# Performance work log

Measured on AMD Instinct MI355X. Metric: run time of the kernel, lower is better.

The kernel has to match this reference:

```python
import jax, jax.numpy as jnp
import numpy as np

HS = 512

def setup_inputs() -> dict:
    key = jax.random.key(0)
    k1, k2, k3, k4 = jax.random.split(key, 4)
    B, T, D = 128, 1024, 256
    x = jax.random.normal(k1, (B, T, D), dtype=jnp.float32)
    # init like torch.Tensor (uninitialized) -> use small random values for a usable baseline
    W = jax.random.normal(k2, (D, 4 * HS), dtype=jnp.float32) * (1.0 / np.sqrt(D))
    U = jax.random.normal(k3, (HS, 4 * HS), dtype=jnp.float32) * (1.0 / np.sqrt(HS))
    bias = jax.random.normal(k4, (4 * HS,), dtype=jnp.float32) * 0.01
    return {"x": x, "W": W, "U": U, "bias": bias}

def reference(x, W, U, bias):
    B = x.shape[0]
    h0 = jnp.zeros((B, HS), dtype=x.dtype)
    c0 = jnp.zeros((B, HS), dtype=x.dtype)
    # precompute input projection for all timesteps (same math, hoisted out of recurrence)
    xW = jnp.einsum('btd,dg->btg', x, W) + bias  # [B, T, 4*HS]

    def step(carry, xw_t):
        h_t, c_t = carry
        gates = xw_t + h_t @ U  # [B, 4*HS]
        i_t = jax.nn.sigmoid(gates[:, :HS])
        f_t = jax.nn.sigmoid(gates[:, HS:2 * HS])
        g_t = jnp.tanh(gates[:, 2 * HS:3 * HS])
        o_t = jax.nn.sigmoid(gates[:, 3 * HS:])
        c_t = f_t * c_t + i_t * g_t
        h_t = o_t * jnp.tanh(c_t)
        return (h_t, c_t), h_t

    (h_T, c_T), hs = jax.lax.scan(step, (h0, c0), jnp.swapaxes(xW, 0, 1))
    hidden_sequence = jnp.swapaxes(hs, 0, 1)  # [B, T, HS]
    return hidden_sequence, (h_T, c_T)
```

## Files before the change

### kernel.cpp

```cpp
#include <hip/hip_runtime.h>

typedef __attribute__((ext_vector_type(8))) short short8;
typedef __attribute__((ext_vector_type(4))) float floatx4;

#define B_   128
#define T_   1024
#define D_   256
#define HS_  512
#define NKT  24

#define OFF_X   0ull
#define SZ_X    ((size_t)B_*T_*D_*2)
#define OFF_W   (OFF_X + SZ_X)
#define SZ_W    ((size_t)16*4*48*64*8*2)
#define OFF_H   (OFF_W + SZ_W)
#define SZ_H    ((size_t)2*B_*HS_*2)
#define OFF_C   (OFF_H + SZ_H)

__device__ inline unsigned short f2bf(float f){
  union { float f; unsigned u; } v; v.f = f;
  unsigned r = v.u + 0x7FFFu + ((v.u >> 16) & 1u);
  return (unsigned short)(r >> 16);
}

__global__ void k_zero(unsigned* __restrict__ hbuf32, unsigned* __restrict__ cnt32){
  int i = blockIdx.x*256 + threadIdx.x;
  if (i < (int)(SZ_H/4)) hbuf32[i] = 0u;
  if (i < 512)           cnt32[i]  = 0u;
}

__global__ void k_convx(const float* __restrict__ x, unsigned short* __restrict__ xb){
  size_t i = ((size_t)blockIdx.x*256 + threadIdx.x)*8;
  const float* s = x + i;
  short8 r;
#pragma unroll
  for (int j=0;j<8;j++) r[j] = (short)f2bf(s[j]);
  *(short8*)(void*)(xb + i) = r;
}

__global__ void k_wfrag(const float* __restrict__ W, const float* __restrict__ U,
                        unsigned short* __restrict__ wf){
  int flat = blockIdx.x*256 + threadIdx.x;
  int lane = flat & 63;
  int rest = flat >> 6;
  int nt   = rest & 1;
  int kt   = (rest >> 1) % 24;
  int sw   = (rest >> 1) / 24;
  int w    = sw & 3;
  int sub  = sw >> 2;
  int colg  = w*HS_ + sub*32 + nt*16 + (lane & 15);
  int kbase = kt*32 + (lane >> 4)*8;
  short8 r;
#pragma unroll
  for (int j=0;j<8;j++){
    int k = kbase + j;
    float v = (k < D_) ? W[(size_t)k*2048 + colg] : U[(size_t)(k-D_)*2048 + colg];
    r[j] = (short)f2bf(v);
  }
  *(short8*)(void*)(wf + (size_t)flat*8) = r;
}

__global__ __launch_bounds__(256, 1) void k_lstm(
  const unsigned short* __restrict__ xb,
  const unsigned short* __restrict__ wf,
  const float* __restrict__ bias,
  unsigned short* __restrict__ hbuf,
  unsigned int* __restrict__ cnt,
  float* __restrict__ out)
{
  __shared__ unsigned short A_lds[NKT*64*8];
  __shared__ float g_lds[4][16][34];

  const int wg   = blockIdx.x;
  const int group = wg >> 4, sub = wg & 15;
  const int tid  = threadIdx.x;
  const int wave = tid >> 6, lane = tid & 63;

  short8 bw[48];
  {
    const unsigned short* wp = wf + (size_t)(sub*4 + wave)*48*512 + (size_t)lane*8;
#pragma unroll
    for (int i=0;i<48;i++) bw[i] = *(const short8*)(const void*)(wp + i*512);
  }

  const int row_e = tid >> 4;
  const int cp    = (tid & 15)*2;
  float bres[8];
#pragma unroll
  for (int q=0;q<4;q++)
#pragma unroll
    for (int e=0;e<2;e++)
      bres[q*2+e] = bias[q*HS_ + sub*32 + cp + e];

  float c0 = 0.f, c1 = 0.f;
  unsigned int* mycnt = cnt + group*64;
  const size_t HSQ = (size_t)B_*T_*HS_;
  const int grow = group*16 + row_e;
  const int gcol = sub*32 + cp;

  const int xrow0 = (tid >> 5);
  const int xkc   = (tid & 31);
  short8 xr0, xr1;
  {
    const unsigned short* s0 = xb + ((size_t)(group*16 + xrow0)*T_ + 0)*D_ + xkc*8;
    const unsigned short* s1 = xb + ((size_t)(group*16 + xrow0 + 8)*T_ + 0)*D_ + xkc*8;
    xr0 = *(const short8*)(const void*)s0;
    xr1 = *(const short8*)(const void*)s1;
  }

  for (int t=0; t<T_; ++t){
    {
      int kt = xkc >> 2, quad = xkc & 3;
      *(short8*)(void*)&A_lds[((kt*64) + quad*16 + xrow0    )*8] = xr0;
      *(short8*)(void*)&A_lds[((kt*64) + quad*16 + xrow0 + 8)*8] = xr1;
    }
    const unsigned short* hsrc = hbuf + (size_t)(t & 1)*B_*HS_;
#pragma unroll
    for (int j=0;j<8;j++){
      int id  = j*256 + tid;
      int row = id >> 7;
      int hc  = id & 127;
      unsigned long long v = __hip_atomic_load(
        (const unsigned long long*)(const void*)(hsrc + (size_t)(group*16+row)*HS_ + hc*4),
        __ATOMIC_RELAXED, __HIP_MEMORY_SCOPE_AGENT);
      int kt = 8 + (hc >> 3), quad = (hc >> 1) & 3, off = (hc & 1)*4;
      *(unsigned long long*)(void*)&A_lds[(kt*64 + quad*16 + row)*8 + off] = v;
    }
    __syncthreads();

    floatx4 acc0 = {0.f,0.f,0.f,0.f}, acc1 = {0.f,0.f,0.f,0.f};
#pragma unroll
    for (int kt=0; kt<NKT; ++kt){
      short8 a = *(const short8*)(const void*)&A_lds[(kt*64 + lane)*8];
      acc0 = __builtin_amdgcn_mfma_f32_16x16x32_bf16(a, bw[kt*2+0], acc0, 0,0,0);
      acc1 = __builtin_amdgcn_mfma_f32_16x16x32_bf16(a, bw[kt*2+1], acc1, 0,0,0);
    }
#pragma unroll
    for (int r=0;r<4;r++){
      int row = (lane>>4)*4 + r;
      g_lds[wave][row][(lane&15)]    = acc0[r];
      g_lds[wave][row][16+(lane&15)] = acc1[r];
    }
    __syncthreads();

    float hv0, hv1;
    {
      float gi = g_lds[0][row_e][cp]   + bres[0];
      float gf = g_lds[1][row_e][cp]   + bres[2];
      float gg = g_lds[2][row_e][cp]   + bres[4];
      float go = g_lds[3][row_e][cp]   + bres[6];
      float i_ = 1.f/(1.f + __expf(-gi));
      float f_ = 1.f/(1.f + __expf(-gf));
      float g_ = 1.f - 2.f/(__expf(2.f*gg)+1.f);
      float o_ = 1.f/(1.f + __expf(-go));
      c0 = f_*c0 + i_*g_;
      hv0 = o_*(1.f - 2.f/(__expf(2.f*c0)+1.f));
    }
    {
      float gi = g_lds[0][row_e][cp+1] + bres[1];
      float gf = g_lds[1][row_e][cp+1] + bres[3];
      float gg = g_lds[2][row_e][cp+1] + bres[5];
      float go = g_lds[3][row_e][cp+1] + bres[7];
      float i_ = 1.f/(1.f + __expf(-gi));
      float f_ = 1.f/(1.f + __expf(-gf));
      float g_ = 1.f - 2.f/(__expf(2.f*gg)+1.f);
      float o_ = 1.f/(1.f + __expf(-go));
      c1 = f_*c1 + i_*g_;
      hv1 = o_*(1.f - 2.f/(__expf(2.f*c1)+1.f));
    }

    float2 h2; h2.x = hv0; h2.y = hv1;
    *(float2*)(out + ((size_t)grow*T_ + t)*HS_ + gcol) = h2;
    unsigned short* hdst = hbuf + (size_t)((t+1)&1)*B_*HS_ + (size_t)grow*HS_ + gcol;
    __hip_atomic_store((unsigned int*)(void*)hdst,
                       (unsigned)f2bf(hv0) | ((unsigned)f2bf(hv1) << 16),
                       __ATOMIC_RELAXED, __HIP_MEMORY_SCOPE_AGENT);
    if (t == T_-1){
      *(float2*)(out + HSQ + (size_t)grow*HS_ + gcol) = h2;
      float2 cc; cc.x = c0; cc.y = c1;
      *(float2*)(out + HSQ + (size_t)B_*HS_ + (size_t)grow*HS_ + gcol) = cc;
    }

    __syncthreads();
    if (tid == 0){
      __atomic_signal_fence(__ATOMIC_RELEASE);
      __hip_atomic_fetch_add(mycnt, 1u, __ATOMIC_RELAXED, __HIP_MEMORY_SCOPE_AGENT);
    }
    if (t+1 < T_){
      const unsigned short* s0 = xb + ((size_t)(group*16 + xrow0)*T_ + (t+1))*D_ + xkc*8;
      const unsigned short* s1 = xb + ((size_t)(group*16 + xrow0 + 8)*T_ + (t+1))*D_ + xkc*8;
      xr0 = *(const short8*)(const void*)s0;
      xr1 = *(const short8*)(const void*)s1;
    }
    if (tid == 0){
      unsigned tgt = 16u*(unsigned)(t+1);
      while (__hip_atomic_load(mycnt, __ATOMIC_RELAXED, __HIP_MEMORY_SCOPE_AGENT) < tgt)
        __builtin_amdgcn_s_sleep(1);
      __atomic_signal_fence(__ATOMIC_ACQUIRE);
    }
    __syncthreads();
  }
}

extern "C" void kernel_launch(void* const* d_in, const int* in_sizes, int n_in,
                              void* d_out, int out_size, void* d_ws, size_t ws_size,
                              hipStream_t stream){
  (void)in_sizes; (void)n_in; (void)out_size; (void)ws_size;
  const float* x    = (const float*)d_in[0];
  const float* W    = (const float*)d_in[1];
  const float* U    = (const float*)d_in[2];
  const float* bias = (const float*)d_in[3];
  char* ws = (char*)d_ws;
  unsigned short* xb = (unsigned short*)(ws + OFF_X);
  unsigned short* wf = (unsigned short*)(ws + OFF_W);
  unsigned short* hb = (unsigned short*)(ws + OFF_H);
  unsigned int*   cn = (unsigned int*)(ws + OFF_C);
  float* out = (float*)d_out;

  hipLaunchKernelGGL(k_zero,  dim3(256),   dim3(256), 0, stream, (unsigned*)hb, cn);
  hipLaunchKernelGGL(k_convx, dim3((B_*T_*D_/8)/256), dim3(256), 0, stream, x, xb);
  hipLaunchKernelGGL(k_wfrag, dim3(768),   dim3(256), 0, stream, W, U, wf);
  hipLaunchKernelGGL(k_lstm,  dim3(128),   dim3(256), 0, stream, xb, wf, bias, hb, cn, out);
}
```

Measured before the change: 4.745 ms.

## Restructure LSTM step: per-wave flags, register x operands, in-wave gate math

Replaces the single atomic counter plus tid-0 spin and block barriers with per-wave step flags that every wave polls directly, so a wave waits only on flag values. The x-projection operands are now loaded straight into registers one step ahead and their MFMAs are issued before the h exchange, overlapping input compute with the cross-block wait. Weight columns are permuted so each wave holds matching i/f/g/o gate columns, letting gate nonlinearities and the cell update run in registers with lane shuffles instead of through an LDS gate buffer and an extra barrier. The h tile in LDS uses an XOR swizzle to avoid bank conflicts, and the time loop is unrolled by two with ping-pong x buffers, at the cost of more register pressure and more complex memory-ordering logic.

```diff
diff --git a/kernel.cpp b/kernel.cpp
--- a/kernel.cpp
+++ b/kernel.cpp
@@ -7,7 +7,6 @@
 #define T_   1024
 #define D_   256
 #define HS_  512
-#define NKT  24
 
 #define OFF_X   0ull
 #define SZ_X    ((size_t)B_*T_*D_*2)
@@ -48,7 +47,8 @@
   int sw   = (rest >> 1) / 24;
   int w    = sw & 3;
   int sub  = sw >> 2;
-  int colg  = w*HS_ + sub*32 + nt*16 + (lane & 15);
+  int gate = nt*2 + ((lane >> 3) & 1);
+  int colg = gate*HS_ + sub*32 + w*8 + (lane & 7);
   int kbase = kt*32 + (lane >> 4)*8;
   short8 r;
 #pragma unroll
@@ -65,16 +65,16 @@
   const unsigned short* __restrict__ wf,
   const float* __restrict__ bias,
   unsigned short* __restrict__ hbuf,
-  unsigned int* __restrict__ cnt,
+  unsigned int* __restrict__ flags,
   float* __restrict__ out)
 {
-  __shared__ unsigned short A_lds[NKT*64*8];
-  __shared__ float g_lds[4][16][34];
-
-  const int wg   = blockIdx.x;
+  __shared__ unsigned short A_lds[16*512];
+
+  const int wg    = blockIdx.x;
   const int group = wg >> 4, sub = wg & 15;
-  const int tid  = threadIdx.x;
-  const int wave = tid >> 6, lane = tid & 63;
+  const int tid   = threadIdx.x;
+  const int wave  = tid >> 6, lane = tid & 63;
+  const int g16   = group*16;
 
   short8 bw[48];
   {
@@ -83,123 +83,121 @@
     for (int i=0;i<48;i++) bw[i] = *(const short8*)(const void*)(wp + i*512);
   }
 
-  const int row_e = tid >> 4;
-  const int cp    = (tid & 15)*2;
-  float bres[8];
-#pragma unroll
-  for (int q=0;q<4;q++)
-#pragma unroll
-    for (int e=0;e<2;e++)
-      bres[q*2+e] = bias[q*HS_ + sub*32 + cp + e];
-
-  float c0 = 0.f, c1 = 0.f;
-  unsigned int* mycnt = cnt + group*64;
+  const int bit3 = (lane >> 3) & 1;
+  const int hcol = sub*32 + wave*8 + (lane & 7);
+  const int r0   = (lane >> 4) * 4;
+  const float b0 = bias[bit3*HS_ + hcol];
+  const float b1 = bias[(2+bit3)*HS_ + hcol];
+
+  const int arow = lane & 15, aq = lane >> 4;
+  const unsigned short* xbase = xb + ((size_t)(g16 + arow)*T_)*D_ + aq*8;
+  const int se = (aq*16 + (arow ^ (aq<<1)      ))*8;
+  const int so = (aq*16 + (arow ^ ((aq<<1)|1)  ))*8;
+
+  const int hc    = tid & 127;
+  const int kt_l  = hc >> 3, qs = (hc >> 1) & 3, half = hc & 1;
+  const int es    = (qs << 1) | (kt_l & 1);
+  const int rbase = tid >> 7;
+
+  unsigned int* myflags = flags + group*64;
   const size_t HSQ = (size_t)B_*T_*HS_;
-  const int grow = group*16 + row_e;
-  const int gcol = sub*32 + cp;
-
-  const int xrow0 = (tid >> 5);
-  const int xkc   = (tid & 31);
-  short8 xr0, xr1;
-  {
-    const unsigned short* s0 = xb + ((size_t)(group*16 + xrow0)*T_ + 0)*D_ + xkc*8;
-    const unsigned short* s1 = xb + ((size_t)(group*16 + xrow0 + 8)*T_ + 0)*D_ + xkc*8;
-    xr0 = *(const short8*)(const void*)s0;
-    xr1 = *(const short8*)(const void*)s1;
+
+  float cc[4] = {0.f,0.f,0.f,0.f};
+
+  short8 xfA[8], xfB[8];
+#pragma unroll
+  for (int kt=0;kt<8;kt++) xfA[kt] = *(const short8*)(const void*)(xbase + kt*32);
+
+#define LSTM_STEP(TT, XC, XN) {                                                \
+                     \
+  if ((TT) > 0){                                                               \
+    unsigned fv;                                                               \
+    do { fv = __hip_atomic_load(myflags + lane, __ATOMIC_RELAXED,              \
+                                __HIP_MEMORY_SCOPE_AGENT);                     \
+    } while (!__all((int)(fv >= (unsigned)(TT))));                             \
+    __atomic_signal_fence(__ATOMIC_ACQUIRE);                                   \
+  }                                                                            \
+                                    \
+  const unsigned short* hsrc = hbuf + (size_t)((TT)&1)*B_*HS_;                 \
+  unsigned long long hv[8];                                                    \
+  _Pragma("unroll")                                                            \
+  for (int j=0;j<8;j++)                                                        \
+    hv[j] = __hip_atomic_load(                                                 \
+      (const unsigned long long*)(const void*)(hsrc +                          \
+        (size_t)(g16 + 2*j + rbase)*HS_ + hc*4),                               \
+      __ATOMIC_RELAXED, __HIP_MEMORY_SCOPE_AGENT);                             \
+                \
+  { int tn = (TT)+1 < T_ ? (TT)+1 : T_-1;                                      \
+    const unsigned short* xp = xbase + (size_t)tn*D_;                          \
+    _Pragma("unroll")                                                          \
+    for (int kt=0;kt<8;kt++) XN[kt] = *(const short8*)(const void*)(xp+kt*32); \
+  }                                                                            \
+                 \
+  floatx4 acc0 = {0.f,0.f,0.f,0.f}, acc1 = {0.f,0.f,0.f,0.f};                  \
+  _Pragma("unroll")                                                            \
+  for (int kt=0;kt<8;kt++){                                                    \
+    acc0 = __builtin_amdgcn_mfma_f32_16x16x32_bf16(XC[kt], bw[kt*2+0], acc0, 0,0,0); \
+    acc1 = __builtin_amdgcn_mfma_f32_16x16x32_bf16(XC[kt], bw[kt*2+1], acc1, 0,0,0); \
+  }                                                                            \
+                       \
+  _Pragma("unroll")                                                            \
+  for (int j=0;j<8;j++){                                                       \
+    int row = 2*j + rbase;                                                     \
+    *(unsigned long long*)(void*)&A_lds[kt_l*512 + (qs*16 + (row ^ es))*8      \
+                                        + half*4] = hv[j];                     \
+  }                                                                            \
+  asm volatile("s_waitcnt lgkmcnt(0)" ::: "memory");                           \
+  __builtin_amdgcn_s_barrier();                                                \
+  asm volatile("" ::: "memory");                                               \
+                                                   \
+  _Pragma("unroll")                                                            \
+  for (int kt=0;kt<16;kt++){                                                   \
+    short8 a = *(const short8*)(const void*)&A_lds[kt*512 + ((kt&1) ? so : se)]; \
+    acc0 = __builtin_amdgcn_mfma_f32_16x16x32_bf16(a, bw[(8+kt)*2+0], acc0, 0,0,0); \
+    acc1 = __builtin_amdgcn_mfma_f32_16x16x32_bf16(a, bw[(8+kt)*2+1], acc1, 0,0,0); \
+  }                                                                            \
+   \
+  unsigned short* hdst = hbuf + (size_t)(((TT)+1)&1)*B_*HS_;                   \
+  _Pragma("unroll")                                                            \
+  for (int r=0;r<4;r++){                                                       \
+    float a0 = acc0[r] + b0;                                                   \
+    float a1 = acc1[r] + b1;                                                   \
+    float s0 = 1.f/(1.f + __expf(-a0));                   \
+    float e1 = __expf(bit3 ? -a1 : 2.f*a1);                                    \
+    float s1 = bit3 ? 1.f/(1.f+e1) : 1.f - 2.f/(e1+1.f);   \
+    float p  = s0 * s1;                                     \
+    float pr = __shfl_xor(p, 8, 64);                                           \
+    cc[r] = s0*cc[r] + pr;                            \
+    float th = 1.f - 2.f/(__expf(2.f*cc[r])+1.f);                              \
+    float hval = s1 * th;                             \
+    float hprt = __shfl_xor(hval, 1, 64);            \
+    int gr = g16 + r0 + r;                                                     \
+    if ((lane & 9) == 8){      \
+      unsigned pk = (unsigned)f2bf(hval) | ((unsigned)f2bf(hprt) << 16);       \
+      __hip_atomic_store((unsigned int*)(void*)(hdst + (size_t)gr*HS_ + hcol), \
+                         pk, __ATOMIC_RELAXED, __HIP_MEMORY_SCOPE_AGENT);      \
+    }                                                                          \
+    if (lane & 8){                                                             \
+      out[((size_t)gr*T_ + (TT))*HS_ + hcol] = hval;                           \
+      if ((TT) == T_-1){                                                       \
+        out[HSQ + (size_t)gr*HS_ + hcol] = hval;                               \
+        out[HSQ + (size_t)B_*HS_ + (size_t)gr*HS_ + hcol] = cc[r];             \
+      }                                                                        \
+    }                                                                          \
+  }                                                                            \
+             \
+  __atomic_signal_fence(__ATOMIC_RELEASE);                                     \
+  asm volatile("s_waitcnt vmcnt(0)" ::: "memory");                             \
+  if (lane == 0)                                                               \
+    __hip_atomic_store(myflags + (sub*4 + wave), (unsigned)((TT)+1),           \
+                       __ATOMIC_RELAXED, __HIP_MEMORY_SCOPE_AGENT);            \
+}
+
+  for (int t=0; t<T_; t+=2){
+    LSTM_STEP(t,   xfA, xfB);
+    LSTM_STEP(t+1, xfB, xfA);
   }
-
-  for (int t=0; t<T_; ++t){
-    {
-      int kt = xkc >> 2, quad = xkc & 3;
-      *(short8*)(void*)&A_lds[((kt*64) + quad*16 + xrow0    )*8] = xr0;
-      *(short8*)(void*)&A_lds[((kt*64) + quad*16 + xrow0 + 8)*8] = xr1;
-    }
-    const unsigned short* hsrc = hbuf + (size_t)(t & 1)*B_*HS_;
-#pragma unroll
-    for (int j=0;j<8;j++){
-      int id  = j*256 + tid;
-      int row = id >> 7;
-      int hc  = id & 127;
-      unsigned long long v = __hip_atomic_load(
-        (const unsigned long long*)(const void*)(hsrc + (size_t)(group*16+row)*HS_ + hc*4),
-        __ATOMIC_RELAXED, __HIP_MEMORY_SCOPE_AGENT);
-      int kt = 8 + (hc >> 3), quad = (hc >> 1) & 3, off = (hc & 1)*4;
-      *(unsigned long long*)(void*)&A_lds[(kt*64 + quad*16 + row)*8 + off] = v;
-    }
-    __syncthreads();
-
-    floatx4 acc0 = {0.f,0.f,0.f,0.f}, acc1 = {0.f,0.f,0.f,0.f};
-#pragma unroll
-    for (int kt=0; kt<NKT; ++kt){
-      short8 a = *(const short8*)(const void*)&A_lds[(kt*64 + lane)*8];
-      acc0 = __builtin_amdgcn_mfma_f32_16x16x32_bf16(a, bw[kt*2+0], acc0, 0,0,0);
-      acc1 = __builtin_amdgcn_mfma_f32_16x16x32_bf16(a, bw[kt*2+1], acc1, 0,0,0);
-    }
-#pragma unroll
-    for (int r=0;r<4;r++){
-      int row = (lane>>4)*4 + r;
-      g_lds[wave][row][(lane&15)]    = acc0[r];
-      g_lds[wave][row][16+(lane&15)] = acc1[r];
-    }
-    __syncthreads();
-
-    float hv0, hv1;
-    {
-      float gi = g_lds[0][row_e][cp]   + bres[0];
-      float gf = g_lds[1][row_e][cp]   + bres[2];
-      float gg = g_lds[2][row_e][cp]   + bres[4];
-      float go = g_lds[3][row_e][cp]   + bres[6];
-      float i_ = 1.f/(1.f + __expf(-gi));
-      float f_ = 1.f/(1.f + __expf(-gf));
-      float g_ = 1.f - 2.f/(__expf(2.f*gg)+1.f);
-      float o_ = 1.f/(1.f + __expf(-go));
-      c0 = f_*c0 + i_*g_;
-      hv0 = o_*(1.f - 2.f/(__expf(2.f*c0)+1.f));
-    }
-    {
-      float gi = g_lds[0][row_e][cp+1] + bres[1];
-      float gf = g_lds[1][row_e][cp+1] + bres[3];
-      float gg = g_lds[2][row_e][cp+1] + bres[5];
-      float go = g_lds[3][row_e][cp+1] + bres[7];
-      float i_ = 1.f/(1.f + __expf(-gi));
-      float f_ = 1.f/(1.f + __expf(-gf));
-      float g_ = 1.f - 2.f/(__expf(2.f*gg)+1.f);
-      float o_ = 1.f/(1.f + __expf(-go));
-      c1 = f_*c1 + i_*g_;
-      hv1 = o_*(1.f - 2.f/(__expf(2.f*c1)+1.f));
-    }
-
-    float2 h2; h2.x = hv0; h2.y = hv1;
-    *(float2*)(out + ((size_t)grow*T_ + t)*HS_ + gcol) = h2;
-    unsigned short* hdst = hbuf + (size_t)((t+1)&1)*B_*HS_ + (size_t)grow*HS_ + gcol;
-    __hip_atomic_store((unsigned int*)(void*)hdst,
-                       (unsigned)f2bf(hv0) | ((unsigned)f2bf(hv1) << 16),
-                       __ATOMIC_RELAXED, __HIP_MEMORY_SCOPE_AGENT);
-    if (t == T_-1){
-      *(float2*)(out + HSQ + (size_t)grow*HS_ + gcol) = h2;
-      float2 cc; cc.x = c0; cc.y = c1;
-      *(float2*)(out + HSQ + (size_t)B_*HS_ + (size_t)grow*HS_ + gcol) = cc;
-    }
-
-    __syncthreads();
-    if (tid == 0){
-      __atomic_signal_fence(__ATOMIC_RELEASE);
-      __hip_atomic_fetch_add(mycnt, 1u, __ATOMIC_RELAXED, __HIP_MEMORY_SCOPE_AGENT);
-    }
-    if (t+1 < T_){
-      const unsigned short* s0 = xb + ((size_t)(group*16 + xrow0)*T_ + (t+1))*D_ + xkc*8;
-      const unsigned short* s1 = xb + ((size_t)(group*16 + xrow0 + 8)*T_ + (t+1))*D_ + xkc*8;
-      xr0 = *(const short8*)(const void*)s0;
-      xr1 = *(const short8*)(const void*)s1;
-    }
-    if (tid == 0){
-      unsigned tgt = 16u*(unsigned)(t+1);
-      while (__hip_atomic_load(mycnt, __ATOMIC_RELAXED, __HIP_MEMORY_SCOPE_AGENT) < tgt)
-        __builtin_amdgcn_s_sleep(1);
-      __atomic_signal_fence(__ATOMIC_ACQUIRE);
-    }
-    __syncthreads();
-  }
+#undef LSTM_STEP
 }
 
 extern "C" void kernel_launch(void* const* d_in, const int* in_sizes, int n_in,
@@ -212,13 +210,13 @@
   const float* bias = (const float*)d_in[3];
   char* ws = (char*)d_ws;
   unsigned short* xb = (unsigned short*)(ws + OFF_X);
-  unsigned short* wf = (unsigned short*)(ws + OFF_W);
+  unsigned short* wfp= (unsigned short*)(ws + OFF_W);
   unsigned short* hb = (unsigned short*)(ws + OFF_H);
-  unsigned int*   cn = (unsigned int*)(ws + OFF_C);
+  unsigned int*   fl = (unsigned int*)(ws + OFF_C);
   float* out = (float*)d_out;
 
-  hipLaunchKernelGGL(k_zero,  dim3(256),   dim3(256), 0, stream, (unsigned*)hb, cn);
+  hipLaunchKernelGGL(k_zero,  dim3(256),   dim3(256), 0, stream, (unsigned*)hb, fl);
   hipLaunchKernelGGL(k_convx, dim3((B_*T_*D_/8)/256), dim3(256), 0, stream, x, xb);
-  hipLaunchKernelGGL(k_wfrag, dim3(768),   dim3(256), 0, stream, W, U, wf);
-  hipLaunchKernelGGL(k_lstm,  dim3(128),   dim3(256), 0, stream, xb, wf, bias, hb, cn, out);
-}
+  hipLaunchKernelGGL(k_wfrag, dim3(768),   dim3(256), 0, stream, W, U, wfp);
+  hipLaunchKernelGGL(k_lstm,  dim3(128),   dim3(256), 0, stream, xb, wfp, bias, hb, fl, out);
+}
```

Result: slower. 5.956 ms (+25.5%).
